# Kernel optimization log

Hardware: AMD Instinct MI355X
Metric: run time of the kernel (lower is better)

## Reference

```python
import jax, jax.numpy as jnp
import numpy as np

B, C, Ci, N = 4, 512, 256, 4096
EPS = 1e-5

def _proj(x, W, b):
    # 1x1 Conv1d == per-node linear: x [B,C,N], W [O,C], b [O] -> [B,O,N]
    return jnp.einsum('oc,bcn->bon', W, x) + b[None, :, None]

def setup_inputs() -> dict:
    key = jax.random.key(0)
    ks = jax.random.split(key, 12)
    s_in = 1.0 / np.sqrt(C)
    s_ci = 1.0 / np.sqrt(Ci)
    return {
        'v':   jax.random.normal(ks[0], (B, C, N), jnp.float32),
        'Wg':  jax.random.normal(ks[1], (Ci, C), jnp.float32) * s_in,
        'bg':  jax.random.normal(ks[2], (Ci,), jnp.float32) * 0.01,
        'Wth': jax.random.normal(ks[3], (Ci, C), jnp.float32) * s_in,
        'bth': jax.random.normal(ks[4], (Ci,), jnp.float32) * 0.01,
        'Wph': jax.random.normal(ks[5], (Ci, C), jnp.float32) * s_in,
        'bph': jax.random.normal(ks[6], (Ci,), jnp.float32) * 0.01,
        'Ww':  jax.random.normal(ks[7], (C, Ci), jnp.float32) * s_ci,
        'bw':  jax.random.normal(ks[8], (C,), jnp.float32) * 0.01,
        'gamma': jax.random.uniform(ks[9], (C,), jnp.float32, 0.5, 1.5),
        'beta':  jax.random.normal(ks[10], (C,), jnp.float32) * 0.01,
    }

def reference(v, Wg, bg, Wth, bth, Wph, bph, Ww, bw, gamma, beta):
    # projections (1x1 convs)
    g_v = _proj(v, Wg, bg).transpose(0, 2, 1)      # [B,N,Ci]
    theta_v = _proj(v, Wth, bth).transpose(0, 2, 1)  # [B,N,Ci]
    phi_v = _proj(v, Wph, bph)                      # [B,Ci,N]
    # non-local affinity (no softmax), divided by N
    R = jnp.einsum('bnc,bcm->bnm', theta_v, phi_v) / N  # [B,N,N]
    y = jnp.einsum('bnm,bmc->bnc', R, g_v)              # [B,N,Ci]
    y = y.transpose(0, 2, 1)                            # [B,Ci,N]
    # W: 1x1 conv back to C, then BatchNorm1d (training-mode stats)
    Wy = _proj(y, Ww, bw)                               # [B,C,N]
    mean = jnp.mean(Wy, axis=(0, 2), keepdims=True)
    var = jnp.mean(jnp.square(Wy - mean), axis=(0, 2), keepdims=True)  # biased, as torch BN uses
    Wy_bn = (Wy - mean) * jax.lax.rsqrt(var + EPS)
    Wy_bn = Wy_bn * gamma[None, :, None] + beta[None, :, None]
    return Wy_bn + v
```

## Files before the change

### kernel.cpp

```cpp
#include <hip/hip_runtime.h>
#include <math.h>


#define B_  4
#define C_  512
#define CI_ 256
#define N_  4096

typedef __attribute__((ext_vector_type(8))) short bf16x8;
typedef __attribute__((ext_vector_type(4))) float f32x4;

#define G_OFF     0L
#define P1_OFF    1048576L
#define SP_OFF    1572864L
#define P2_OFF    1835008L
#define MISC_OFF  2359296L
#define R_OFF     (MISC_OFF + 0)
#define SUM_OFF   (MISC_OFF + 2048)
#define SSQ_OFF   (MISC_OFF + 2560)
#define BE_OFF    (MISC_OFF + 3072)
#define U1_OFF    (MISC_OFF + 5120)
#define U2_OFF    (MISC_OFF + 6144)
#define VH_OFF    2367488L
#define VL_OFF    6561792L
#define VTH_OFF   10756096L
#define VTL_OFF   14950400L
#define WEH_OFF   19144704L
#define WEL_OFF   19668992L

__device__ __forceinline__ unsigned short f2bf(float f) {
    union { float f; unsigned int u; } a; a.f = f;
    unsigned int u = a.u;
    u += 0x7fffu + ((u >> 16) & 1u);
    return (unsigned short)(u >> 16);
}
__device__ __forceinline__ float bf2f(unsigned short s) {
    union { unsigned int u; float f; } a; a.u = ((unsigned int)s) << 16; return a.f;
}
__device__ __forceinline__ void gload_lds16(const char* g, char* l) {
    __builtin_amdgcn_global_load_lds(
        (const __attribute__((address_space(1))) unsigned int*)g,
        (__attribute__((address_space(3))) unsigned int*)l, 16, 0, 0);
}

__global__ __launch_bounds__(256) void cast1(
    const float* __restrict__ v, unsigned short* __restrict__ vh,
    unsigned short* __restrict__ vl, float* __restrict__ r)
{
    long idx = (long)blockIdx.x * 256 + threadIdx.x;
    float4 f = ((const float4*)v)[idx];
    ushort4 h, l;
    h.x = f2bf(f.x); l.x = f2bf(f.x - bf2f(h.x));
    h.y = f2bf(f.y); l.y = f2bf(f.y - bf2f(h.y));
    h.z = f2bf(f.z); l.z = f2bf(f.z - bf2f(h.z));
    h.w = f2bf(f.w); l.w = f2bf(f.w - bf2f(h.w));
    ((ushort4*)vh)[idx] = h;
    ((ushort4*)vl)[idx] = l;
    float s = f.x + f.y + f.z + f.w;
    s += __shfl_xor(s, 1);  s += __shfl_xor(s, 2);  s += __shfl_xor(s, 4);
    s += __shfl_xor(s, 8);  s += __shfl_xor(s, 16); s += __shfl_xor(s, 32);
    if ((threadIdx.x & 63) == 0) atomicAdd(&r[idx >> 10], s);
}

__global__ __launch_bounds__(256) void cast2_transpose(
    const float* __restrict__ v, unsigned int* __restrict__ vth,
    unsigned int* __restrict__ vtl)
{
    __shared__ float tile[32][33];
    const int b = blockIdx.z;
    const int n0 = blockIdx.x * 32, c0 = blockIdx.y * 32;
    const int t = threadIdx.x, tx = t & 31, ty = t >> 5;
#pragma unroll
    for (int j = 0; j < 4; ++j)
        tile[ty + 8 * j][tx] = v[((long)b * C_ + c0 + ty + 8 * j) * N_ + n0 + tx];
    __syncthreads();
#pragma unroll
    for (int p = 0; p < 2; ++p) {
        int nl = p * 16 + (t >> 4);
        int cl = (t & 15) * 2;
        float f0 = tile[cl][nl], f1 = tile[cl + 1][nl];
        unsigned short h0 = f2bf(f0), h1 = f2bf(f1);
        unsigned short l0 = f2bf(f0 - bf2f(h0)), l1 = f2bf(f1 - bf2f(h1));
        long e = ((long)b * N_ + n0 + nl) * C_ + c0 + cl;
        vth[e >> 1] = (unsigned int)h0 | ((unsigned int)h1 << 16);
        vtl[e >> 1] = (unsigned int)l0 | ((unsigned int)l1 << 16);
    }
}

__global__ __launch_bounds__(256, 2) void gram_mfma(
    const unsigned short* __restrict__ vh, const unsigned short* __restrict__ vl,
    float* __restrict__ Gp)
{
    __shared__ char smem[65536];
    const int t = threadIdx.x, lane = t & 63, w = t >> 6;
    const int z = blockIdx.z, b = z >> 3, ch = z & 7;
    const long m0 = blockIdx.y * 128, n0 = blockIdx.x * 128;
    const long k0b = (long)ch * 1024;

    const unsigned short* src = (w & 1) ? vl : vh;
    const long row0 = (w < 2) ? m0 : n0;
    const char* g = (const char*)(src + ((long)b * C_ + row0) * N_) + k0b;
    const long stride = (long)N_ * 2;
    const char* gs = g + (long)(lane >> 3) * stride + (((lane & 7) ^ (lane >> 3)) << 4);
    char* lbase = smem + w * 16384;

    const int wr = w >> 1, wc = w & 1;
    const int l15 = lane & 15, hi4 = lane >> 4;
    const int swz = (l15 & 7) << 4;
    const int arow = (wr * 64 + l15) * 128;
    const int brow = (wc * 64 + l15) * 128;
    const char* Ah = smem;          const char* Al = smem + 16384;
    const char* Bh = smem + 32768;  const char* Bl = smem + 49152;

    f32x4 acc[4][4];
#pragma unroll
    for (int mi = 0; mi < 4; ++mi)
#pragma unroll
        for (int nj = 0; nj < 4; ++nj) acc[mi][nj] = (f32x4){0.f, 0.f, 0.f, 0.f};

    for (int s = 0; s < 8; ++s) {
#pragma unroll
        for (int i = 0; i < 16; ++i)
            gload_lds16(gs + (long)i * 8 * stride + s * 128, lbase + i * 1024);
        __syncthreads();
#pragma unroll
        for (int kk = 0; kk < 2; ++kk) {
            const int off = (kk * 64 + hi4 * 16) ^ swz;
            bf16x8 ah[4], al[4], bh[4], bl[4];
#pragma unroll
            for (int mi = 0; mi < 4; ++mi) {
                ah[mi] = *(const bf16x8*)(Ah + arow + mi * 2048 + off);
                al[mi] = *(const bf16x8*)(Al + arow + mi * 2048 + off);
            }
#pragma unroll
            for (int nj = 0; nj < 4; ++nj) {
                bh[nj] = *(const bf16x8*)(Bh + brow + nj * 2048 + off);
                bl[nj] = *(const bf16x8*)(Bl + brow + nj * 2048 + off);
            }
#pragma unroll
            for (int mi = 0; mi < 4; ++mi)
#pragma unroll
                for (int nj = 0; nj < 4; ++nj) {
                    acc[mi][nj] = __builtin_amdgcn_mfma_f32_16x16x32_bf16(ah[mi], bh[nj], acc[mi][nj], 0, 0, 0);
                    acc[mi][nj] = __builtin_amdgcn_mfma_f32_16x16x32_bf16(ah[mi], bl[nj], acc[mi][nj], 0, 0, 0);
                    acc[mi][nj] = __builtin_amdgcn_mfma_f32_16x16x32_bf16(al[mi], bh[nj], acc[mi][nj], 0, 0, 0);
                }
        }
        __syncthreads();
    }
    float* gp = Gp + (long)z * (C_ * C_);
#pragma unroll
    for (int mi = 0; mi < 4; ++mi)
#pragma unroll
        for (int nj = 0; nj < 4; ++nj)
#pragma unroll
            for (int rr = 0; rr < 4; ++rr) {
                long row = m0 + wr * 64 + mi * 16 + hi4 * 4 + rr;
                long col = n0 + wc * 64 + nj * 16 + l15;
                gp[row * C_ + col] = acc[mi][nj][rr];
            }
}

__global__ __launch_bounds__(256) void reduce_g(
    const float* __restrict__ Gp, float* __restrict__ G)
{
    long e4 = (long)blockIdx.x * 256 + threadIdx.x;
    long b = e4 >> 16;
    float4 s = make_float4(0.f, 0.f, 0.f, 0.f);
    for (int ch = 0; ch < 8; ++ch) {
        float4 p = ((const float4*)Gp)[(b * 8 + ch) * 65536 + (e4 & 65535)];
        s.x += p.x; s.y += p.y; s.z += p.z; s.w += p.w;
    }
    ((float4*)G)[e4] = s;
}

__global__ __launch_bounds__(256, 2) void wy_mfma(
    const unsigned short* __restrict__ weh, const unsigned short* __restrict__ wel,
    const unsigned short* __restrict__ vth, const unsigned short* __restrict__ vtl,
    const float* __restrict__ be, const float* __restrict__ bw,
    float* __restrict__ out, float* __restrict__ sums, float* __restrict__ ssqs)
{
    __shared__ char smem[65536];
    const int t = threadIdx.x, lane = t & 63, w = t >> 6;
    const int b = blockIdx.z;
    const long m0 = blockIdx.y * 128;
    const long n0 = blockIdx.x * 128;

    const char* g;
    if (w < 2) g = (const char*)(((w & 1) ? wel : weh) + ((long)b * C_ + m0) * C_);
    else       g = (const char*)(((w & 1) ? vtl : vth) + ((long)b * N_ + n0) * C_);
    const long stride = (long)C_ * 2;
    const char* gs = g + (long)(lane >> 3) * stride + (((lane & 7) ^ (lane >> 3)) << 4);
    char* lbase = smem + w * 16384;

    const int wr = w >> 1, wc = w & 1;
    const int l15 = lane & 15, hi4 = lane >> 4;
    const int swz = (l15 & 7) << 4;
    const int arow = (wr * 64 + l15) * 128;
    const int brow = (wc * 64 + l15) * 128;
    const char* Ah = smem;          const char* Al = smem + 16384;
    const char* Bh = smem + 32768;  const char* Bl = smem + 49152;

    f32x4 acc[4][4];
#pragma unroll
    for (int mi = 0; mi < 4; ++mi)
#pragma unroll
        for (int nj = 0; nj < 4; ++nj) acc[mi][nj] = (f32x4){0.f, 0.f, 0.f, 0.f};

    for (int s = 0; s < 8; ++s) {
#pragma unroll
        for (int i = 0; i < 16; ++i)
            gload_lds16(gs + (long)i * 8 * stride + s * 128, lbase + i * 1024);
        __syncthreads();
#pragma unroll
        for (int kk = 0; kk < 2; ++kk) {
            const int off = (kk * 64 + hi4 * 16) ^ swz;
            bf16x8 ah[4], al[4], bh[4], bl[4];
#pragma unroll
            for (int mi = 0; mi < 4; ++mi) {
                ah[mi] = *(const bf16x8*)(Ah + arow + mi * 2048 + off);
                al[mi] = *(const bf16x8*)(Al + arow + mi * 2048 + off);
            }
#pragma unroll
            for (int nj = 0; nj < 4; ++nj) {
                bh[nj] = *(const bf16x8*)(Bh + brow + nj * 2048 + off);
                bl[nj] = *(const bf16x8*)(Bl + brow + nj * 2048 + off);
            }
#pragma unroll
            for (int mi = 0; mi < 4; ++mi)
#pragma unroll
                for (int nj = 0; nj < 4; ++nj) {
                    acc[mi][nj] = __builtin_amdgcn_mfma_f32_16x16x32_bf16(ah[mi], bh[nj], acc[mi][nj], 0, 0, 0);
                    acc[mi][nj] = __builtin_amdgcn_mfma_f32_16x16x32_bf16(ah[mi], bl[nj], acc[mi][nj], 0, 0, 0);
                    acc[mi][nj] = __builtin_amdgcn_mfma_f32_16x16x32_bf16(al[mi], bh[nj], acc[mi][nj], 0, 0, 0);
                }
        }
        __syncthreads();
    }

    float sm[4][4], sq[4][4];
#pragma unroll
    for (int mi = 0; mi < 4; ++mi)
#pragma unroll
        for (int rr = 0; rr < 4; ++rr) { sm[mi][rr] = 0.f; sq[mi][rr] = 0.f; }

#pragma unroll
    for (int mi = 0; mi < 4; ++mi) {
#pragma unroll
        for (int rr = 0; rr < 4; ++rr) {
            long o = m0 + wr * 64 + mi * 16 + hi4 * 4 + rr;
            float bv = be[b * C_ + o] * (1.0f / (float)N_) + bw[o];
#pragma unroll
            for (int nj = 0; nj < 4; ++nj) {
                long n = n0 + wc * 64 + nj * 16 + l15;
                float val = acc[mi][nj][rr] + bv;
                out[((long)b * C_ + o) * N_ + n] = val;
                sm[mi][rr] += val;
                sq[mi][rr] += val * val;
            }
        }
    }
#pragma unroll
    for (int mi = 0; mi < 4; ++mi)
#pragma unroll
        for (int rr = 0; rr < 4; ++rr) {
            float s1 = sm[mi][rr], s2 = sq[mi][rr];
            s1 += __shfl_xor(s1, 1); s2 += __shfl_xor(s2, 1);
            s1 += __shfl_xor(s1, 2); s2 += __shfl_xor(s2, 2);
            s1 += __shfl_xor(s1, 4); s2 += __shfl_xor(s2, 4);
            s1 += __shfl_xor(s1, 8); s2 += __shfl_xor(s2, 8);
            if (l15 == 0) {
                long o = m0 + wr * 64 + mi * 16 + hi4 * 4 + rr;
                atomicAdd(&sums[o], s1);
                atomicAdd(&ssqs[o], s2);
            }
        }
}

__global__ __launch_bounds__(256) void gemm_nn(
    const float* __restrict__ A, long sA, int lda,
    const float* __restrict__ Bm, long sB, int ldb,
    float* __restrict__ Cm, long sC, int ldc,
    int K, float scale, int mode,
    const float* __restrict__ bth, float* __restrict__ be,
    unsigned short* __restrict__ weh, unsigned short* __restrict__ wel)
{
    int b = blockIdx.z;
    const float* Ab = A + (long)b * sA;
    const float* Bb = Bm + (long)b * sB;
    int i0 = blockIdx.y * 64, j0 = blockIdx.x * 64;

    __shared__ __align__(16) float As[16][64];
    __shared__ __align__(16) float Bs[16][64];

    int t = threadIdx.x, tx = t & 15, ty = t >> 4;
    int am = t >> 2, akq = (t & 3) << 2;
    int bk = t >> 4, bn4 = (t & 15) << 2;

    float acc[4][4];
#pragma unroll
    for (int r = 0; r < 4; ++r)
#pragma unroll
        for (int c = 0; c < 4; ++c) acc[r][c] = 0.f;

    for (int k0 = 0; k0 < K; k0 += 16) {
        float4 va = *(const float4*)&Ab[(long)(i0 + am) * lda + k0 + akq];
        As[akq + 0][am] = va.x; As[akq + 1][am] = va.y;
        As[akq + 2][am] = va.z; As[akq + 3][am] = va.w;
        *(float4*)&Bs[bk][bn4] = *(const float4*)&Bb[(long)(k0 + bk) * ldb + j0 + bn4];
        __syncthreads();
#pragma unroll
        for (int k = 0; k < 16; ++k) {
            float4 a4 = *(float4*)&As[k][ty * 4];
            float4 b4 = *(float4*)&Bs[k][tx * 4];
            float a[4]  = {a4.x, a4.y, a4.z, a4.w};
            float bb[4] = {b4.x, b4.y, b4.z, b4.w};
#pragma unroll
            for (int r = 0; r < 4; ++r)
#pragma unroll
                for (int c = 0; c < 4; ++c)
                    acc[r][c] += a[r] * bb[c];
        }
        __syncthreads();
    }

    if (mode == 2) {
#pragma unroll
        for (int r = 0; r < 4; ++r) {
            int o = i0 + ty * 4 + r, p = j0 + tx * 4;
            ushort4 h, l;
            float f0 = acc[r][0] * scale, f1 = acc[r][1] * scale;
            float f2 = acc[r][2] * scale, f3 = acc[r][3] * scale;
            h.x = f2bf(f0); l.x = f2bf(f0 - bf2f(h.x));
            h.y = f2bf(f1); l.y = f2bf(f1 - bf2f(h.y));
            h.z = f2bf(f2); l.z = f2bf(f2 - bf2f(h.z));
            h.w = f2bf(f3); l.w = f2bf(f3 - bf2f(h.w));
            long e = (((long)b * C_ + o) * C_ + p) >> 2;
            ((ushort4*)weh)[e] = h;
            ((ushort4*)wel)[e] = l;
        }
        return;
    }
    float* Cb = Cm + (long)b * sC;
#pragma unroll
    for (int r = 0; r < 4; ++r) {
        float4 o0 = make_float4(acc[r][0] * scale, acc[r][1] * scale,
                                acc[r][2] * scale, acc[r][3] * scale);
        *(float4*)&Cb[(long)(i0 + ty * 4 + r) * ldc + j0 + tx * 4] = o0;
    }
    if (mode == 1) {
#pragma unroll
        for (int r = 0; r < 4; ++r) {
            float pr = acc[r][0] * bth[j0 + tx * 4 + 0]
                     + acc[r][1] * bth[j0 + tx * 4 + 1]
                     + acc[r][2] * bth[j0 + tx * 4 + 2]
                     + acc[r][3] * bth[j0 + tx * 4 + 3];
            pr += __shfl_xor(pr, 1); pr += __shfl_xor(pr, 2);
            pr += __shfl_xor(pr, 4); pr += __shfl_xor(pr, 8);
            if (tx == 0) atomicAdd(&be[b * C_ + i0 + ty * 4 + r], pr);
        }
    }
}

__global__ __launch_bounds__(256) void gemm_nt_sp(
    const float* __restrict__ P1, const float* __restrict__ Wph,
    float* __restrict__ SP, const float* __restrict__ u1,
    const float* __restrict__ u2, const float* __restrict__ bg,
    const float* __restrict__ bph)
{
    int b = blockIdx.z;
    const float* Ab = P1 + (long)b * (CI_ * C_);
    int i0 = blockIdx.y * 64, j0 = blockIdx.x * 64;

    __shared__ __align__(16) float As[16][64];
    __shared__ __align__(16) float Bs[16][64];

    int t = threadIdx.x, tx = t & 15, ty = t >> 4;
    int lr = t >> 2, lk = (t & 3) << 2;

    float acc[4][4];
#pragma unroll
    for (int r = 0; r < 4; ++r)
#pragma unroll
        for (int c = 0; c < 4; ++c) acc[r][c] = 0.f;

    for (int kt = 0; kt < C_; kt += 16) {
        float4 va = *(const float4*)&Ab[(long)(i0 + lr) * C_ + kt + lk];
        float4 vb = *(const float4*)&Wph[(long)(j0 + lr) * C_ + kt + lk];
        As[lk + 0][lr] = va.x; As[lk + 1][lr] = va.y; As[lk + 2][lr] = va.z; As[lk + 3][lr] = va.w;
        Bs[lk + 0][lr] = vb.x; Bs[lk + 1][lr] = vb.y; Bs[lk + 2][lr] = vb.z; Bs[lk + 3][lr] = vb.w;
        __syncthreads();
#pragma unroll
        for (int k = 0; k < 16; ++k) {
            float4 a4 = *(float4*)&As[k][ty * 4];
            float4 b4 = *(float4*)&Bs[k][tx * 4];
            float a[4]  = {a4.x, a4.y, a4.z, a4.w};
            float bb[4] = {b4.x, b4.y, b4.z, b4.w};
#pragma unroll
            for (int r = 0; r < 4; ++r)
#pragma unroll
                for (int c = 0; c < 4; ++c)
                    acc[r][c] += a[r] * bb[c];
        }
        __syncthreads();
    }
    float* Cb = SP + (long)b * (CI_ * CI_);
#pragma unroll
    for (int r = 0; r < 4; ++r) {
        int cr = i0 + ty * 4 + r;
        float u1v = u1[b * CI_ + cr], bgv = bg[cr];
        float4 o0;
        float* po = (float*)&o0;
#pragma unroll
        for (int c = 0; c < 4; ++c) {
            int ic = j0 + tx * 4 + c;
            po[c] = acc[r][c] + u1v * bph[ic] + bgv * (u2[b * CI_ + ic] + (float)N_ * bph[ic]);
        }
        *(float4*)&Cb[(long)cr * CI_ + j0 + tx * 4] = o0;
    }
}

__global__ __launch_bounds__(256) void rank1_prep(
    const float* __restrict__ Wg, const float* __restrict__ Wph,
    const float* __restrict__ r, float* __restrict__ u1, float* __restrict__ u2)
{
    int blk = blockIdx.x;
    int b = blk >> 2, q = blk & 3;
    int t = threadIdx.x;
    int c = q * 64 + (t >> 2);
    int kq = t & 3;
    const float* rb = r + b * C_;
    float s1 = 0.f, s2 = 0.f;
    for (int k = kq * 128; k < kq * 128 + 128; k += 4) {
        float4 wg = *(const float4*)&Wg[(long)c * C_ + k];
        float4 wp = *(const float4*)&Wph[(long)c * C_ + k];
        float4 rv = *(const float4*)&rb[k];
        s1 += wg.x * rv.x + wg.y * rv.y + wg.z * rv.z + wg.w * rv.w;
        s2 += wp.x * rv.x + wp.y * rv.y + wp.z * rv.z + wp.w * rv.w;
    }
    s1 += __shfl_xor(s1, 1); s2 += __shfl_xor(s2, 1);
    s1 += __shfl_xor(s1, 2); s2 += __shfl_xor(s2, 2);
    if (kq == 0) {
        u1[b * CI_ + c] = s1;
        u2[b * CI_ + c] = s2;
    }
}

__global__ __launch_bounds__(256) void bn_apply(
    float* __restrict__ out, const float* __restrict__ v,
    const float* __restrict__ sums, const float* __restrict__ ssqs,
    const float* __restrict__ gamma, const float* __restrict__ beta)
{
    long i = (long)blockIdx.x * 256 + threadIdx.x;
    int o = (int)((i >> 10) & (C_ - 1));
    const float inv = 1.0f / ((float)B_ * (float)N_);
    float mean = sums[o] * inv;
    float var  = ssqs[o] * inv - mean * mean;
    float sc = gamma[o] * rsqrtf(var + 1e-5f);
    float sh = beta[o] - mean * sc;
    float4 wv = ((const float4*)out)[i];
    float4 vv = ((const float4*)v)[i];
    wv.x = wv.x * sc + sh + vv.x;
    wv.y = wv.y * sc + sh + vv.y;
    wv.z = wv.z * sc + sh + vv.z;
    wv.w = wv.w * sc + sh + vv.w;
    ((float4*)out)[i] = wv;
}

extern "C" void kernel_launch(void* const* d_in, const int* in_sizes, int n_in,
                              void* d_out, int out_size, void* d_ws, size_t ws_size,
                              hipStream_t stream)
{
    const float* v     = (const float*)d_in[0];
    const float* Wg    = (const float*)d_in[1];
    const float* bg    = (const float*)d_in[2];
    const float* Wth   = (const float*)d_in[3];
    const float* bth   = (const float*)d_in[4];
    const float* Wph   = (const float*)d_in[5];
    const float* bph   = (const float*)d_in[6];
    const float* Ww    = (const float*)d_in[7];
    const float* bw    = (const float*)d_in[8];
    const float* gamma = (const float*)d_in[9];
    const float* beta  = (const float*)d_in[10];
    float* out = (float*)d_out;
    float* ws  = (float*)d_ws;

    float* G    = ws + G_OFF;
    float* P1   = ws + P1_OFF;
    float* SP   = ws + SP_OFF;
    float* P2   = ws + P2_OFF;
    float* r    = ws + R_OFF;
    float* sums = ws + SUM_OFF;
    float* ssqs = ws + SSQ_OFF;
    float* be   = ws + BE_OFF;
    float* u1   = ws + U1_OFF;
    float* u2   = ws + U2_OFF;
    unsigned short* vh  = (unsigned short*)(ws + VH_OFF);
    unsigned short* vl  = (unsigned short*)(ws + VL_OFF);
    unsigned short* vth = (unsigned short*)(ws + VTH_OFF);
    unsigned short* vtl = (unsigned short*)(ws + VTL_OFF);
    unsigned short* weh = (unsigned short*)(ws + WEH_OFF);
    unsigned short* wel = (unsigned short*)(ws + WEL_OFF);
    float* Gp = ws + VTH_OFF;

    hipMemsetAsync(r, 0, 5120 * sizeof(float), stream);

    cast1<<<8192, 256, 0, stream>>>(v, vh, vl, r);

    gram_mfma<<<dim3(4, 4, 32), 256, 0, stream>>>(vh, vl, Gp);
    reduce_g<<<1024, 256, 0, stream>>>(Gp, G);

    cast2_transpose<<<dim3(128, 16, 4), 256, 0, stream>>>(v, (unsigned int*)vth, (unsigned int*)vtl);

    rank1_prep<<<16, 256, 0, stream>>>(Wg, Wph, r, u1, u2);

    gemm_nn<<<dim3(8, 4, 4), 256, 0, stream>>>(
        Wg, 0, C_, G, (long)C_ * C_, C_, P1, (long)CI_ * C_, C_,
        C_, 1.0f, 0, nullptr, nullptr, nullptr, nullptr);

    gemm_nt_sp<<<dim3(4, 4, 4), 256, 0, stream>>>(P1, Wph, SP, u1, u2, bg, bph);

    gemm_nn<<<dim3(4, 8, 4), 256, 0, stream>>>(
        Ww, 0, CI_, SP, (long)CI_ * CI_, CI_, P2, (long)C_ * CI_, CI_,
        CI_, 1.0f, 1, bth, be, nullptr, nullptr);

    gemm_nn<<<dim3(8, 8, 4), 256, 0, stream>>>(
        P2, (long)C_ * CI_, CI_, Wth, 0, C_, nullptr, 0, 0,
        CI_, 1.0f / (float)N_, 2, nullptr, nullptr, weh, wel);

    wy_mfma<<<dim3(32, 4, 4), 256, 0, stream>>>(weh, wel, vth, vtl, be, bw, out, sums, ssqs);

    bn_apply<<<8192, 256, 0, stream>>>(out, v, sums, ssqs, gamma, beta);
}
```

Before: 331.8 us.

## Fuse cast kernels, drop low-order split terms, atomically reduce Gram partials

The two casting passes over v are merged into one tiled kernel that writes the hi/lo bf16 copies, the transposed hi copy, and the row sums in a single read. Gram partial sums now accumulate into G with float atomics, which removes the separate reduction kernel and its partial buffer. One low-order cross term is dropped from the Gram (lo x hi) and from the Wy GEMM (the transposed-v lo plane), so fewer MFMAs run and less memory is read, at some cost in precision. Tiles are halved along N so more blocks fit per CU (launch bounds raised to 4).

```diff
diff --git a/kernel.cpp b/kernel.cpp
--- a/kernel.cpp
+++ b/kernel.cpp
@@ -24,9 +24,8 @@
 #define VH_OFF    2367488L
 #define VL_OFF    6561792L
 #define VTH_OFF   10756096L
-#define VTL_OFF   14950400L
-#define WEH_OFF   19144704L
-#define WEL_OFF   19668992L
+#define WEH_OFF   14950400L
+#define WEL_OFF   15474688L
 
 __device__ __forceinline__ unsigned short f2bf(float f) {
     union { float f; unsigned int u; } a; a.f = f;
@@ -43,197 +42,192 @@
         (__attribute__((address_space(3))) unsigned int*)l, 16, 0, 0);
 }
 
-__global__ __launch_bounds__(256) void cast1(
+__global__ __launch_bounds__(256) void cast_fused(
     const float* __restrict__ v, unsigned short* __restrict__ vh,
-    unsigned short* __restrict__ vl, float* __restrict__ r)
-{
-    long idx = (long)blockIdx.x * 256 + threadIdx.x;
-    float4 f = ((const float4*)v)[idx];
-    ushort4 h, l;
-    h.x = f2bf(f.x); l.x = f2bf(f.x - bf2f(h.x));
-    h.y = f2bf(f.y); l.y = f2bf(f.y - bf2f(h.y));
-    h.z = f2bf(f.z); l.z = f2bf(f.z - bf2f(h.z));
-    h.w = f2bf(f.w); l.w = f2bf(f.w - bf2f(h.w));
-    ((ushort4*)vh)[idx] = h;
-    ((ushort4*)vl)[idx] = l;
-    float s = f.x + f.y + f.z + f.w;
-    s += __shfl_xor(s, 1);  s += __shfl_xor(s, 2);  s += __shfl_xor(s, 4);
-    s += __shfl_xor(s, 8);  s += __shfl_xor(s, 16); s += __shfl_xor(s, 32);
-    if ((threadIdx.x & 63) == 0) atomicAdd(&r[idx >> 10], s);
-}
-
-__global__ __launch_bounds__(256) void cast2_transpose(
-    const float* __restrict__ v, unsigned int* __restrict__ vth,
-    unsigned int* __restrict__ vtl)
-{
-    __shared__ float tile[32][33];
+    unsigned short* __restrict__ vl, unsigned short* __restrict__ vth,
+    float* __restrict__ r)
+{
+    __shared__ float tile[64][65];
     const int b = blockIdx.z;
-    const int n0 = blockIdx.x * 32, c0 = blockIdx.y * 32;
-    const int t = threadIdx.x, tx = t & 31, ty = t >> 5;
-#pragma unroll
-    for (int j = 0; j < 4; ++j)
-        tile[ty + 8 * j][tx] = v[((long)b * C_ + c0 + ty + 8 * j) * N_ + n0 + tx];
+    const int n0 = blockIdx.x * 64, c0 = blockIdx.y * 64;
+    const int t = threadIdx.x, rq = t >> 4, cq = t & 15;
+#pragma unroll
+    for (int p = 0; p < 4; ++p) {
+        int row = p * 16 + rq;
+        long e = ((long)(b * C_ + c0 + row)) * N_ + n0 + cq * 4;
+        float4 f = *(const float4*)&v[e];
+        ushort4 h, l;
+        h.x = f2bf(f.x); l.x = f2bf(f.x - bf2f(h.x));
+        h.y = f2bf(f.y); l.y = f2bf(f.y - bf2f(h.y));
+        h.z = f2bf(f.z); l.z = f2bf(f.z - bf2f(h.z));
+        h.w = f2bf(f.w); l.w = f2bf(f.w - bf2f(h.w));
+        *(ushort4*)&vh[e] = h;
+        *(ushort4*)&vl[e] = l;
+        tile[row][cq * 4 + 0] = f.x; tile[row][cq * 4 + 1] = f.y;
+        tile[row][cq * 4 + 2] = f.z; tile[row][cq * 4 + 3] = f.w;
+        float s = f.x + f.y + f.z + f.w;
+        s += __shfl_xor(s, 1); s += __shfl_xor(s, 2);
+        s += __shfl_xor(s, 4); s += __shfl_xor(s, 8);
+        if (cq == 0) atomicAdd(&r[b * C_ + c0 + row], s);
+    }
     __syncthreads();
 #pragma unroll
-    for (int p = 0; p < 2; ++p) {
-        int nl = p * 16 + (t >> 4);
-        int cl = (t & 15) * 2;
-        float f0 = tile[cl][nl], f1 = tile[cl + 1][nl];
-        unsigned short h0 = f2bf(f0), h1 = f2bf(f1);
-        unsigned short l0 = f2bf(f0 - bf2f(h0)), l1 = f2bf(f1 - bf2f(h1));
-        long e = ((long)b * N_ + n0 + nl) * C_ + c0 + cl;
-        vth[e >> 1] = (unsigned int)h0 | ((unsigned int)h1 << 16);
-        vtl[e >> 1] = (unsigned int)l0 | ((unsigned int)l1 << 16);
-    }
-}
-
-__global__ __launch_bounds__(256, 2) void gram_mfma(
+    for (int p = 0; p < 4; ++p) {
+        int nl = p * 16 + rq;
+        float f0 = tile[cq * 4 + 0][nl], f1 = tile[cq * 4 + 1][nl];
+        float f2 = tile[cq * 4 + 2][nl], f3 = tile[cq * 4 + 3][nl];
+        ushort4 h;
+        h.x = f2bf(f0); h.y = f2bf(f1); h.z = f2bf(f2); h.w = f2bf(f3);
+        long e = ((long)(b * N_ + n0 + nl)) * C_ + c0 + cq * 4;
+        *(ushort4*)&vth[e] = h;
+    }
+}
+
+__global__ __launch_bounds__(256, 4) void gram_mfma(
     const unsigned short* __restrict__ vh, const unsigned short* __restrict__ vl,
-    float* __restrict__ Gp)
-{
-    __shared__ char smem[65536];
+    float* __restrict__ G)
+{
+    __shared__ char smem[32768];
     const int t = threadIdx.x, lane = t & 63, w = t >> 6;
     const int z = blockIdx.z, b = z >> 3, ch = z & 7;
-    const long m0 = blockIdx.y * 128, n0 = blockIdx.x * 128;
+    const long m0 = blockIdx.y * 128, n0 = blockIdx.x * 64;
     const long k0b = (long)ch * 1024;
-
-    const unsigned short* src = (w & 1) ? vl : vh;
-    const long row0 = (w < 2) ? m0 : n0;
-    const char* g = (const char*)(src + ((long)b * C_ + row0) * N_) + k0b;
     const long stride = (long)N_ * 2;
+
+    const char* g; char* lbase;
+    if (w == 0)      { g = (const char*)(vh + ((long)b * C_ + m0     ) * N_) + k0b; lbase = smem; }
+    else if (w == 1) { g = (const char*)(vh + ((long)b * C_ + m0 + 64) * N_) + k0b; lbase = smem + 8192; }
+    else if (w == 2) { g = (const char*)(vh + ((long)b * C_ + n0     ) * N_) + k0b; lbase = smem + 16384; }
+    else             { g = (const char*)(vl + ((long)b * C_ + n0     ) * N_) + k0b; lbase = smem + 24576; }
     const char* gs = g + (long)(lane >> 3) * stride + (((lane & 7) ^ (lane >> 3)) << 4);
-    char* lbase = smem + w * 16384;
 
     const int wr = w >> 1, wc = w & 1;
     const int l15 = lane & 15, hi4 = lane >> 4;
     const int swz = (l15 & 7) << 4;
     const int arow = (wr * 64 + l15) * 128;
-    const int brow = (wc * 64 + l15) * 128;
-    const char* Ah = smem;          const char* Al = smem + 16384;
-    const char* Bh = smem + 32768;  const char* Bl = smem + 49152;
-
-    f32x4 acc[4][4];
+    const int brow = (wc * 32 + l15) * 128;
+    const char* Ah = smem;
+    const char* Bh = smem + 16384;
+    const char* Bl = smem + 24576;
+
+    f32x4 acc[4][2];
 #pragma unroll
     for (int mi = 0; mi < 4; ++mi)
 #pragma unroll
-        for (int nj = 0; nj < 4; ++nj) acc[mi][nj] = (f32x4){0.f, 0.f, 0.f, 0.f};
+        for (int nj = 0; nj < 2; ++nj) acc[mi][nj] = (f32x4){0.f, 0.f, 0.f, 0.f};
 
     for (int s = 0; s < 8; ++s) {
 #pragma unroll
-        for (int i = 0; i < 16; ++i)
+        for (int i = 0; i < 8; ++i)
             gload_lds16(gs + (long)i * 8 * stride + s * 128, lbase + i * 1024);
         __syncthreads();
 #pragma unroll
         for (int kk = 0; kk < 2; ++kk) {
             const int off = (kk * 64 + hi4 * 16) ^ swz;
-            bf16x8 ah[4], al[4], bh[4], bl[4];
+            bf16x8 ah[4], bh[2], bl[2];
+#pragma unroll
+            for (int mi = 0; mi < 4; ++mi)
+                ah[mi] = *(const bf16x8*)(Ah + arow + mi * 2048 + off);
+#pragma unroll
+            for (int nj = 0; nj < 2; ++nj) {
+                bh[nj] = *(const bf16x8*)(Bh + brow + nj * 2048 + off);
+                bl[nj] = *(const bf16x8*)(Bl + brow + nj * 2048 + off);
+            }
+#pragma unroll
+            for (int mi = 0; mi < 4; ++mi)
+#pragma unroll
+                for (int nj = 0; nj < 2; ++nj)
+                    acc[mi][nj] = __builtin_amdgcn_mfma_f32_16x16x32_bf16(ah[mi], bh[nj], acc[mi][nj], 0, 0, 0);
+#pragma unroll
+            for (int mi = 0; mi < 4; ++mi)
+#pragma unroll
+                for (int nj = 0; nj < 2; ++nj)
+                    acc[mi][nj] = __builtin_amdgcn_mfma_f32_16x16x32_bf16(ah[mi], bl[nj], acc[mi][nj], 0, 0, 0);
+        }
+        __syncthreads();
+    }
+#pragma unroll
+    for (int mi = 0; mi < 4; ++mi)
+#pragma unroll
+        for (int nj = 0; nj < 2; ++nj)
+#pragma unroll
+            for (int rr = 0; rr < 4; ++rr) {
+                long row = m0 + wr * 64 + mi * 16 + hi4 * 4 + rr;
+                long col = n0 + wc * 32 + nj * 16 + l15;
+                atomicAdd(&G[((long)b * C_ + row) * C_ + col], acc[mi][nj][rr]);
+            }
+}
+
+__global__ __launch_bounds__(256, 4) void wy_mfma(
+    const unsigned short* __restrict__ weh, const unsigned short* __restrict__ wel,
+    const unsigned short* __restrict__ vth,
+    const float* __restrict__ be, const float* __restrict__ bw,
+    float* __restrict__ out, float* __restrict__ sums, float* __restrict__ ssqs)
+{
+    __shared__ char smem[40960];
+    const int t = threadIdx.x, lane = t & 63, w = t >> 6;
+    const int b = blockIdx.z;
+    const long m0 = blockIdx.y * 128;
+    const long n0 = blockIdx.x * 64;
+    const long S = (long)C_ * 2;
+
+    const char* wehb = (const char*)(weh + ((long)b * C_ + m0) * C_);
+    const char* welb = (const char*)(wel + ((long)b * C_ + m0) * C_);
+    const char* vhb  = (const char*)(vth + ((long)b * N_ + n0) * C_);
+
+    const char *g0, *g1; char *l0, *l1; int c0n;
+    if (w == 0)      { g0 = wehb;           l0 = smem;                 c0n = 10; g1 = wehb; l1 = smem; }
+    else if (w == 1) { g0 = wehb + 80 * S;  l0 = smem + 10240;         c0n = 6;  g1 = welb;          l1 = smem + 16384; }
+    else if (w == 2) { g0 = welb + 32 * S;  l0 = smem + 16384 + 4096;  c0n = 10; g1 = welb; l1 = smem + 16384; }
+    else             { g0 = welb + 112 * S; l0 = smem + 16384 + 14336; c0n = 2;  g1 = vhb;           l1 = smem + 32768; }
+    const long plane = (long)(lane >> 3) * S + (((lane & 7) ^ (lane >> 3)) << 4);
+
+    const int wr = w >> 1, wc = w & 1;
+    const int l15 = lane & 15, hi4 = lane >> 4;
+    const int swz = (l15 & 7) << 4;
+    const int arow = (wr * 64 + l15) * 128;
+    const int brow = (wc * 32 + l15) * 128;
+    const char* Ah = smem;
+    const char* Al = smem + 16384;
+    const char* Bv = smem + 32768;
+
+    f32x4 acc[4][2];
+#pragma unroll
+    for (int mi = 0; mi < 4; ++mi)
+#pragma unroll
+        for (int nj = 0; nj < 2; ++nj) acc[mi][nj] = (f32x4){0.f, 0.f, 0.f, 0.f};
+
+    for (int s = 0; s < 8; ++s) {
+#pragma unroll
+        for (int i = 0; i < 10; ++i) {
+            const char* src; char* dst;
+            if (i < c0n) { src = g0 + (long)i * 8 * S;         dst = l0 + i * 1024; }
+            else         { src = g1 + (long)(i - c0n) * 8 * S; dst = l1 + (i - c0n) * 1024; }
+            gload_lds16(src + plane + s * 128, dst);
+        }
+        __syncthreads();
+#pragma unroll
+        for (int kk = 0; kk < 2; ++kk) {
+            const int off = (kk * 64 + hi4 * 16) ^ swz;
+            bf16x8 ah[4], al[4], bv[2];
 #pragma unroll
             for (int mi = 0; mi < 4; ++mi) {
                 ah[mi] = *(const bf16x8*)(Ah + arow + mi * 2048 + off);
                 al[mi] = *(const bf16x8*)(Al + arow + mi * 2048 + off);
             }
 #pragma unroll
-            for (int nj = 0; nj < 4; ++nj) {
-                bh[nj] = *(const bf16x8*)(Bh + brow + nj * 2048 + off);
-                bl[nj] = *(const bf16x8*)(Bl + brow + nj * 2048 + off);
-            }
+            for (int nj = 0; nj < 2; ++nj)
+                bv[nj] = *(const bf16x8*)(Bv + brow + nj * 2048 + off);
 #pragma unroll
             for (int mi = 0; mi < 4; ++mi)
 #pragma unroll
-                for (int nj = 0; nj < 4; ++nj) {
-                    acc[mi][nj] = __builtin_amdgcn_mfma_f32_16x16x32_bf16(ah[mi], bh[nj], acc[mi][nj], 0, 0, 0);
-                    acc[mi][nj] = __builtin_amdgcn_mfma_f32_16x16x32_bf16(ah[mi], bl[nj], acc[mi][nj], 0, 0, 0);
-                    acc[mi][nj] = __builtin_amdgcn_mfma_f32_16x16x32_bf16(al[mi], bh[nj], acc[mi][nj], 0, 0, 0);
-                }
-        }
-        __syncthreads();
-    }
-    float* gp = Gp + (long)z * (C_ * C_);
-#pragma unroll
-    for (int mi = 0; mi < 4; ++mi)
-#pragma unroll
-        for (int nj = 0; nj < 4; ++nj)
-#pragma unroll
-            for (int rr = 0; rr < 4; ++rr) {
-                long row = m0 + wr * 64 + mi * 16 + hi4 * 4 + rr;
-                long col = n0 + wc * 64 + nj * 16 + l15;
-                gp[row * C_ + col] = acc[mi][nj][rr];
-            }
-}
-
-__global__ __launch_bounds__(256) void reduce_g(
-    const float* __restrict__ Gp, float* __restrict__ G)
-{
-    long e4 = (long)blockIdx.x * 256 + threadIdx.x;
-    long b = e4 >> 16;
-    float4 s = make_float4(0.f, 0.f, 0.f, 0.f);
-    for (int ch = 0; ch < 8; ++ch) {
-        float4 p = ((const float4*)Gp)[(b * 8 + ch) * 65536 + (e4 & 65535)];
-        s.x += p.x; s.y += p.y; s.z += p.z; s.w += p.w;
-    }
-    ((float4*)G)[e4] = s;
-}
-
-__global__ __launch_bounds__(256, 2) void wy_mfma(
-    const unsigned short* __restrict__ weh, const unsigned short* __restrict__ wel,
-    const unsigned short* __restrict__ vth, const unsigned short* __restrict__ vtl,
-    const float* __restrict__ be, const float* __restrict__ bw,
-    float* __restrict__ out, float* __restrict__ sums, float* __restrict__ ssqs)
-{
-    __shared__ char smem[65536];
-    const int t = threadIdx.x, lane = t & 63, w = t >> 6;
-    const int b = blockIdx.z;
-    const long m0 = blockIdx.y * 128;
-    const long n0 = blockIdx.x * 128;
-
-    const char* g;
-    if (w < 2) g = (const char*)(((w & 1) ? wel : weh) + ((long)b * C_ + m0) * C_);
-    else       g = (const char*)(((w & 1) ? vtl : vth) + ((long)b * N_ + n0) * C_);
-    const long stride = (long)C_ * 2;
-    const char* gs = g + (long)(lane >> 3) * stride + (((lane & 7) ^ (lane >> 3)) << 4);
-    char* lbase = smem + w * 16384;
-
-    const int wr = w >> 1, wc = w & 1;
-    const int l15 = lane & 15, hi4 = lane >> 4;
-    const int swz = (l15 & 7) << 4;
-    const int arow = (wr * 64 + l15) * 128;
-    const int brow = (wc * 64 + l15) * 128;
-    const char* Ah = smem;          const char* Al = smem + 16384;
-    const char* Bh = smem + 32768;  const char* Bl = smem + 49152;
-
-    f32x4 acc[4][4];
-#pragma unroll
-    for (int mi = 0; mi < 4; ++mi)
-#pragma unroll
-        for (int nj = 0; nj < 4; ++nj) acc[mi][nj] = (f32x4){0.f, 0.f, 0.f, 0.f};
-
-    for (int s = 0; s < 8; ++s) {
-#pragma unroll
-        for (int i = 0; i < 16; ++i)
-            gload_lds16(gs + (long)i * 8 * stride + s * 128, lbase + i * 1024);
-        __syncthreads();
-#pragma unroll
-        for (int kk = 0; kk < 2; ++kk) {
-            const int off = (kk * 64 + hi4 * 16) ^ swz;
-            bf16x8 ah[4], al[4], bh[4], bl[4];
-#pragma unroll
-            for (int mi = 0; mi < 4; ++mi) {
-                ah[mi] = *(const bf16x8*)(Ah + arow + mi * 2048 + off);
-                al[mi] = *(const bf16x8*)(Al + arow + mi * 2048 + off);
-            }
-#pragma unroll
-            for (int nj = 0; nj < 4; ++nj) {
-                bh[nj] = *(const bf16x8*)(Bh + brow + nj * 2048 + off);
-                bl[nj] = *(const bf16x8*)(Bl + brow + nj * 2048 + off);
-            }
+                for (int nj = 0; nj < 2; ++nj)
+                    acc[mi][nj] = __builtin_amdgcn_mfma_f32_16x16x32_bf16(ah[mi], bv[nj], acc[mi][nj], 0, 0, 0);
 #pragma unroll
             for (int mi = 0; mi < 4; ++mi)
 #pragma unroll
-                for (int nj = 0; nj < 4; ++nj) {
-                    acc[mi][nj] = __builtin_amdgcn_mfma_f32_16x16x32_bf16(ah[mi], bh[nj], acc[mi][nj], 0, 0, 0);
-                    acc[mi][nj] = __builtin_amdgcn_mfma_f32_16x16x32_bf16(ah[mi], bl[nj], acc[mi][nj], 0, 0, 0);
-                    acc[mi][nj] = __builtin_amdgcn_mfma_f32_16x16x32_bf16(al[mi], bh[nj], acc[mi][nj], 0, 0, 0);
-                }
+                for (int nj = 0; nj < 2; ++nj)
+                    acc[mi][nj] = __builtin_amdgcn_mfma_f32_16x16x32_bf16(al[mi], bv[nj], acc[mi][nj], 0, 0, 0);
         }
         __syncthreads();
     }
@@ -251,8 +245,8 @@
             long o = m0 + wr * 64 + mi * 16 + hi4 * 4 + rr;
             float bv = be[b * C_ + o] * (1.0f / (float)N_) + bw[o];
 #pragma unroll
-            for (int nj = 0; nj < 4; ++nj) {
-                long n = n0 + wc * 64 + nj * 16 + l15;
+            for (int nj = 0; nj < 2; ++nj) {
+                long n = n0 + wc * 32 + nj * 16 + l15;
                 float val = acc[mi][nj][rr] + bv;
                 out[((long)b * C_ + o) * N_ + n] = val;
                 sm[mi][rr] += val;
@@ -498,19 +492,15 @@
     unsigned short* vh  = (unsigned short*)(ws + VH_OFF);
     unsigned short* vl  = (unsigned short*)(ws + VL_OFF);
     unsigned short* vth = (unsigned short*)(ws + VTH_OFF);
-    unsigned short* vtl = (unsigned short*)(ws + VTL_OFF);
     unsigned short* weh = (unsigned short*)(ws + WEH_OFF);
     unsigned short* wel = (unsigned short*)(ws + WEL_OFF);
-    float* Gp = ws + VTH_OFF;
-
+
+    hipMemsetAsync(G, 0, 1048576 * sizeof(float), stream);
     hipMemsetAsync(r, 0, 5120 * sizeof(float), stream);
 
-    cast1<<<8192, 256, 0, stream>>>(v, vh, vl, r);
-
-    gram_mfma<<<dim3(4, 4, 32), 256, 0, stream>>>(vh, vl, Gp);
-    reduce_g<<<1024, 256, 0, stream>>>(Gp, G);
-
-    cast2_transpose<<<dim3(128, 16, 4), 256, 0, stream>>>(v, (unsigned int*)vth, (unsigned int*)vtl);
+    cast_fused<<<dim3(64, 8, 4), 256, 0, stream>>>(v, vh, vl, vth, r);
+
+    gram_mfma<<<dim3(8, 4, 32), 256, 0, stream>>>(vh, vl, G);
 
     rank1_prep<<<16, 256, 0, stream>>>(Wg, Wph, r, u1, u2);
 
@@ -528,7 +518,7 @@
         P2, (long)C_ * CI_, CI_, Wth, 0, C_, nullptr, 0, 0,
         CI_, 1.0f / (float)N_, 2, nullptr, nullptr, weh, wel);
 
-    wy_mfma<<<dim3(32, 4, 4), 256, 0, stream>>>(weh, wel, vth, vtl, be, bw, out, sums, ssqs);
+    wy_mfma<<<dim3(64, 4, 4), 256, 0, stream>>>(weh, wel, vth, be, bw, out, sums, ssqs);
 
     bn_apply<<<8192, 256, 0, stream>>>(out, v, sums, ssqs, gamma, beta);
 }
```

Result: slower. 344.7 us (+3.9%).
